# Performance work log

Hardware: AMD Instinct MI355X
Metric: run time of the kernel (lower is better)

The kernel has to match this reference:

```python
import jax, jax.numpy as jnp
import numpy as np

N_NODES = 50000
N_EDGES = 800000
N_FEAT = 128
HIDDEN = 16
N_CLASSES = 16


def spline_conv(x, src, dst, u, weight, root, bias, num_nodes):
    """SplineConv, dim=1, kernel_size=2, degree=1, open spline, aggr='mean'.

    x: [N, in], weight: [2, in, out], u: [E, 1] pseudo-coords in [0, 1).
    Linear B-spline basis over 2 knots: basis = (1-u, u) -> W[0], W[1].
    Transform at node level first (cheaper than per-edge when E > N),
    then gather along edges and scatter-mean to targets.
    """
    h = jnp.einsum('ni,kio->kno', x, weight)  # [2, N, out]
    msg = (1.0 - u) * h[0][src] + u * h[1][src]  # [E, out]
    agg = jax.ops.segment_sum(msg, dst, num_segments=num_nodes)
    deg = jax.ops.segment_sum(jnp.ones((src.shape[0],), x.dtype), dst,
                              num_segments=num_nodes)
    agg = agg / jnp.maximum(deg, 1.0)[:, None]
    return agg + x @ root + bias


def setup_inputs() -> dict:
    key = jax.random.key(0)
    ks = jax.random.split(key, 8)
    x = jax.random.normal(ks[0], (N_NODES, N_FEAT), dtype=jnp.float32)
    edge_index = jax.random.randint(ks[1], (2, N_EDGES), 0, N_NODES, dtype=jnp.int32)
    edge_attr = jax.random.uniform(ks[2], (N_EDGES, 1), dtype=jnp.float32)
    s1 = 1.0 / np.sqrt(N_FEAT)
    s2 = 1.0 / np.sqrt(HIDDEN)
    return {
        'x': x,
        'edge_index': edge_index,
        'edge_attr': edge_attr,
        'w1': jax.random.normal(ks[3], (2, N_FEAT, HIDDEN), dtype=jnp.float32) * s1,
        'root1': jax.random.normal(ks[4], (N_FEAT, HIDDEN), dtype=jnp.float32) * s1,
        'b1': jnp.zeros((HIDDEN,), dtype=jnp.float32),
        'w2': jax.random.normal(ks[5], (2, HIDDEN, N_CLASSES), dtype=jnp.float32) * s2,
        'root2': jax.random.normal(ks[6], (HIDDEN, N_CLASSES), dtype=jnp.float32) * s2,
        'b2': jnp.zeros((N_CLASSES,), dtype=jnp.float32),
    }


def reference(x, edge_index, edge_attr, w1, root1, b1, w2, root2, b2):
    src, dst = edge_index[0], edge_index[1]
    n = x.shape[0]
    # eval mode: F.dropout(training=False) is identity
    h = jax.nn.elu(spline_conv(x, src, dst, edge_attr, w1, root1, b1, n))
    out = spline_conv(h, src, dst, edge_attr, w2, root2, b2, n)
    return jax.nn.log_softmax(out, axis=1)
```

## Files before the change

kernel.cpp:

```cpp
#include <hip/hip_runtime.h>
#include <hip/hip_bf16.h>
#include <math.h>

#define N_NODES 50000
#define N_EDGES 800000
#define N_FEAT 128
#define HIDDEN 16
#define N_CLASSES 16

#define NBUCK 782
#define PB_NB 196
#define PB_E  4096
#define BCAP  1600

typedef __attribute__((ext_vector_type(8))) short short8v;
typedef __attribute__((ext_vector_type(4))) float floatx4;
typedef __attribute__((ext_vector_type(2))) _Float16 half2v;
typedef __attribute__((ext_vector_type(2))) __fp16 fp16x2;

__device__ __forceinline__ unsigned int f2bf_bits(float f) {
    __hip_bfloat16 h = __float2bfloat16(f);
    return (unsigned int)*reinterpret_cast<unsigned short*>(&h);
}
__device__ __forceinline__ half2v cvt_pk(float a, float b) {
    union { fp16x2 f; half2v h; } x;
    x.f = __builtin_amdgcn_cvt_pkrtz(a, b);
    return x.h;
}
__device__ __forceinline__ half2v uint_as_h2(unsigned int v) {
    union { unsigned int u; half2v h; } x; x.u = v; return x.h;
}
__device__ __forceinline__ unsigned int h2_as_uint(half2v h) {
    union { half2v h; unsigned int u; } x; x.h = h; return x.u;
}


__global__ __launch_bounds__(256) void k_node1(
    const float* __restrict__ x, const float* __restrict__ w1,
    const float* __restrict__ root1, const float* __restrict__ b1,
    unsigned int* __restrict__ ABu, float* __restrict__ C,
    int* __restrict__ rank)
{
    if (threadIdx.x == 0) rank[blockIdx.x] = 0;

    int lane = threadIdx.x & 63;
    int wid  = threadIdx.x >> 6;
    int m = lane & 15;
    int q = lane >> 4;
    int nb = blockIdx.x * 64 + wid * 16;

    short8v bf[3][4];
#pragma unroll
    for (int c = 0; c < 4; ++c) {
        int k0 = c * 32 + q * 8;
        const float* p0 = w1 + (size_t)k0 * 16 + m;
        const float* p1 = w1 + 2048 + (size_t)k0 * 16 + m;
        const float* p2 = root1 + (size_t)k0 * 16 + m;
#pragma unroll
        for (int j = 0; j < 8; ++j) {
            bf[0][c][j] = (short)f2bf_bits(p0[j * 16]);
            bf[1][c][j] = (short)f2bf_bits(p1[j * 16]);
            bf[2][c][j] = (short)f2bf_bits(p2[j * 16]);
        }
    }

    int row = min(nb + m, N_NODES - 1);
    const float* xr = x + (size_t)row * N_FEAT;
    short8v af[4];
#pragma unroll
    for (int c = 0; c < 4; ++c) {
        int k0 = c * 32 + q * 8;
        float4 v0 = *(const float4*)(xr + k0);
        float4 v1 = *(const float4*)(xr + k0 + 4);
        af[c][0] = (short)f2bf_bits(v0.x); af[c][1] = (short)f2bf_bits(v0.y);
        af[c][2] = (short)f2bf_bits(v0.z); af[c][3] = (short)f2bf_bits(v0.w);
        af[c][4] = (short)f2bf_bits(v1.x); af[c][5] = (short)f2bf_bits(v1.y);
        af[c][6] = (short)f2bf_bits(v1.z); af[c][7] = (short)f2bf_bits(v1.w);
    }

    floatx4 acc0 = {0.f, 0.f, 0.f, 0.f};
    floatx4 acc1 = {0.f, 0.f, 0.f, 0.f};
    floatx4 acc2 = {0.f, 0.f, 0.f, 0.f};
#pragma unroll
    for (int c = 0; c < 4; ++c) {
        acc0 = __builtin_amdgcn_mfma_f32_16x16x32_bf16(af[c], bf[0][c], acc0, 0, 0, 0);
        acc1 = __builtin_amdgcn_mfma_f32_16x16x32_bf16(af[c], bf[1][c], acc1, 0, 0, 0);
        acc2 = __builtin_amdgcn_mfma_f32_16x16x32_bf16(af[c], bf[2][c], acc2, 0, 0, 0);
    }

    float bo = b1[m];
#pragma unroll
    for (int j = 0; j < 4; ++j) {
        int n = nb + q * 4 + j;
        if (n < N_NODES) {
            ABu[(size_t)n * 16 + m] = h2_as_uint(cvt_pk(acc0[j], acc1[j]));
            C[(size_t)n * 16 + m] = acc2[j] + bo;
        }
    }
}

__global__ __launch_bounds__(256) void k_part(
    const int* __restrict__ src, const int* __restrict__ dst,
    const float* __restrict__ u, int* __restrict__ rank,
    unsigned int* __restrict__ epr)
{
    __shared__ int cnt[NBUCK];
    for (int i = threadIdx.x; i < NBUCK; i += 256) cnt[i] = 0;
    __syncthreads();
    int ebase = blockIdx.x * PB_E;
    int myd[PB_E / 256];
#pragma unroll
    for (int k = 0; k < PB_E / 256; ++k) {
        int e = ebase + k * 256 + threadIdx.x;
        myd[k] = (e < N_EDGES) ? dst[e] : -1;
        if (myd[k] >= 0) atomicAdd(&cnt[myd[k] >> 6], 1);
    }
    __syncthreads();
    for (int i = threadIdx.x; i < NBUCK; i += 256) {
        int c = cnt[i];
        int base = (c > 0) ? atomicAdd(&rank[i], c) : 0;
        cnt[i] = i * BCAP + base;
    }
    __syncthreads();
#pragma unroll
    for (int k = 0; k < PB_E / 256; ++k) {
        if (myd[k] >= 0) {
            int e = ebase + k * 256 + threadIdx.x;
            int b = myd[k] >> 6;
            int pos = atomicAdd(&cnt[b], 1);
            unsigned int u10 = (unsigned int)(u[e] * 1023.f + 0.5f);
            if (pos < (b + 1) * BCAP)
                epr[pos] = ((unsigned int)src[e] & 0xFFFFu)
                         | (((unsigned int)myd[k] & 63u) << 16)
                         | (u10 << 22);
        }
    }
}

__global__ __launch_bounds__(256) void k_bsort(
    const int* __restrict__ rank, const unsigned int* __restrict__ epr,
    unsigned int* __restrict__ epc, unsigned int* __restrict__ rowpack)
{
    __shared__ unsigned int buf[BCAP];
    __shared__ unsigned int sortc[BCAP];
    __shared__ int cnt[64], cur[64];
    int b = blockIdx.x;
    int beg = b * BCAP;
    int m = min(rank[b], BCAP);

    if (threadIdx.x < 64) cnt[threadIdx.x] = 0;
    __syncthreads();
    for (int i = threadIdx.x; i < m; i += 256) {
        unsigned int p = epr[beg + i];
        buf[i] = p;
        atomicAdd(&cnt[(p >> 16) & 63], 1);
    }
    __syncthreads();
    if (threadIdx.x < 64) {
        int v = cnt[threadIdx.x];
        int s = v;
#pragma unroll
        for (int off = 1; off < 64; off <<= 1) {
            int w = __shfl_up(s, off);
            if (threadIdx.x >= off) s += w;
        }
        int ex = s - v;
        cur[threadIdx.x] = ex;
        int n = (b << 6) + threadIdx.x;
        if (n < N_NODES)
            rowpack[n] = (unsigned int)(beg + ex) | ((unsigned int)v << 21);
    }
    __syncthreads();
    for (int i = threadIdx.x; i < m; i += 256) {
        unsigned int p = buf[i];
        int pos = atomicAdd(&cur[(p >> 16) & 63], 1);
        sortc[pos] = p;
    }
    __syncthreads();
    for (int i = threadIdx.x; i < m; i += 256)
        epc[beg + i] = sortc[i];
}

__global__ __launch_bounds__(256) void k_gfused1(
    const unsigned int* __restrict__ rowpack, const unsigned int* __restrict__ ep,
    const unsigned int* __restrict__ ABu, const float* __restrict__ C,
    const float* __restrict__ w2, const float* __restrict__ root2,
    const float* __restrict__ b2,
    unsigned int* __restrict__ ABu2, float* __restrict__ C2)
{
    __shared__ float W2s[16 * 48];
    for (int t = threadIdx.x; t < 16 * 48; t += 256) {
        int j = t / 48, o = t % 48;
        float v;
        if (o < 16)       v = w2[j * 16 + o];
        else if (o < 32)  v = w2[256 + j * 16 + (o - 16)];
        else              v = root2[j * 16 + (o - 32)];
        W2s[t] = v;
    }
    __syncthreads();

    int n    = (blockIdx.x * 256 + threadIdx.x) >> 6;
    int lane = threadIdx.x & 63;
    int g = lane >> 3;
    int l = lane & 7;
    unsigned int rp = rowpack[n];
    int beg = (int)(rp & 0x1FFFFFu);
    int deg = (int)(rp >> 21);
    int end = beg + deg;
    const uint2* AB2 = (const uint2*)ABu;
    const float uscale = 1.f / 1023.f;
    float ax = 0.f, ay = 0.f;
    int e = beg + g;
    for (; e + 8 < end; e += 16) {
        unsigned int p0 = ep[e];
        unsigned int p1 = ep[e + 8];
        float u0 = (float)(p0 >> 22) * uscale;
        float u1 = (float)(p1 >> 22) * uscale;
        half2v w0 = cvt_pk(1.f - u0, u0);
        half2v w1v = cvt_pk(1.f - u1, u1);
        uint2 q0 = AB2[(size_t)(p0 & 0xFFFF) * 8 + l];
        uint2 q1 = AB2[(size_t)(p1 & 0xFFFF) * 8 + l];
        ax = __builtin_amdgcn_fdot2(w0, uint_as_h2(q0.x), ax, false);
        ay = __builtin_amdgcn_fdot2(w0, uint_as_h2(q0.y), ay, false);
        ax = __builtin_amdgcn_fdot2(w1v, uint_as_h2(q1.x), ax, false);
        ay = __builtin_amdgcn_fdot2(w1v, uint_as_h2(q1.y), ay, false);
    }
    if (e < end) {
        unsigned int p0 = ep[e];
        float u0 = (float)(p0 >> 22) * uscale;
        half2v w0 = cvt_pk(1.f - u0, u0);
        uint2 q0 = AB2[(size_t)(p0 & 0xFFFF) * 8 + l];
        ax = __builtin_amdgcn_fdot2(w0, uint_as_h2(q0.x), ax, false);
        ay = __builtin_amdgcn_fdot2(w0, uint_as_h2(q0.y), ay, false);
    }
#pragma unroll
    for (int s = 8; s < 64; s <<= 1) {
        ax += __shfl_xor(ax, s);
        ay += __shfl_xor(ay, s);
    }
    float dv = fmaxf((float)deg, 1.f);
    float2 cv = *(const float2*)&C[(size_t)n * 16 + 2 * l];
    float pre0 = ax / dv + cv.x;
    float pre1 = ay / dv + cv.y;
    float h0 = pre0 > 0.f ? pre0 : expm1f(pre0);
    float h1 = pre1 > 0.f ? pre1 : expm1f(pre1);

    int oc = (lane < 48) ? lane : 0;
    float val = 0.f;
#pragma unroll
    for (int j2 = 0; j2 < 8; ++j2) {
        float hh0 = __shfl(h0, j2);
        float hh1 = __shfl(h1, j2);
        val += hh0 * W2s[(2 * j2) * 48 + oc] + hh1 * W2s[(2 * j2 + 1) * 48 + oc];
    }
    float bval = __shfl(val, (lane + 16) & 63);
    if (lane < 16)
        ABu2[(size_t)n * 16 + lane] = h2_as_uint(cvt_pk(val, bval));
    else if (lane >= 32 && lane < 48)
        C2[(size_t)n * 16 + (lane - 32)] = val + b2[lane - 32];
}

__global__ __launch_bounds__(256) void k_gather2(
    const unsigned int* __restrict__ rowpack, const unsigned int* __restrict__ ep,
    const unsigned int* __restrict__ ABu, const float* __restrict__ C,
    float* __restrict__ out)
{
    int n    = (blockIdx.x * 256 + threadIdx.x) >> 6;
    int lane = threadIdx.x & 63;
    int g = lane >> 3;
    int l = lane & 7;
    unsigned int rp = rowpack[n];
    int beg = (int)(rp & 0x1FFFFFu);
    int deg = (int)(rp >> 21);
    int end = beg + deg;
    const uint2* AB2 = (const uint2*)ABu;
    const float uscale = 1.f / 1023.f;
    float ax = 0.f, ay = 0.f;
    int e = beg + g;
    for (; e + 8 < end; e += 16) {
        unsigned int p0 = ep[e];
        unsigned int p1 = ep[e + 8];
        float u0 = (float)(p0 >> 22) * uscale;
        float u1 = (float)(p1 >> 22) * uscale;
        half2v w0 = cvt_pk(1.f - u0, u0);
        half2v w1v = cvt_pk(1.f - u1, u1);
        uint2 q0 = AB2[(size_t)(p0 & 0xFFFF) * 8 + l];
        uint2 q1 = AB2[(size_t)(p1 & 0xFFFF) * 8 + l];
        ax = __builtin_amdgcn_fdot2(w0, uint_as_h2(q0.x), ax, false);
        ay = __builtin_amdgcn_fdot2(w0, uint_as_h2(q0.y), ay, false);
        ax = __builtin_amdgcn_fdot2(w1v, uint_as_h2(q1.x), ax, false);
        ay = __builtin_amdgcn_fdot2(w1v, uint_as_h2(q1.y), ay, false);
    }
    if (e < end) {
        unsigned int p0 = ep[e];
        float u0 = (float)(p0 >> 22) * uscale;
        half2v w0 = cvt_pk(1.f - u0, u0);
        uint2 q0 = AB2[(size_t)(p0 & 0xFFFF) * 8 + l];
        ax = __builtin_amdgcn_fdot2(w0, uint_as_h2(q0.x), ax, false);
        ay = __builtin_amdgcn_fdot2(w0, uint_as_h2(q0.y), ay, false);
    }
#pragma unroll
    for (int s = 8; s < 64; s <<= 1) {
        ax += __shfl_xor(ax, s);
        ay += __shfl_xor(ay, s);
    }
    float dv = fmaxf((float)deg, 1.f);
    float2 cv = *(const float2*)&C[(size_t)n * 16 + 2 * l];
    float v0 = ax / dv + cv.x;
    float v1 = ay / dv + cv.y;

    float m = fmaxf(v0, v1);
#pragma unroll
    for (int s = 1; s < 8; s <<= 1) m = fmaxf(m, __shfl_xor(m, s));
    float ssum = __expf(v0 - m) + __expf(v1 - m);
#pragma unroll
    for (int s = 1; s < 8; s <<= 1) ssum += __shfl_xor(ssum, s);
    float lse = m + __logf(ssum);
    if (lane < 8)
        *(float2*)&out[(size_t)n * 16 + 2 * l] = make_float2(v0 - lse, v1 - lse);
}

extern "C" void kernel_launch(void* const* d_in, const int* in_sizes, int n_in,
                              void* d_out, int out_size, void* d_ws, size_t ws_size,
                              hipStream_t stream) {
    const float* x     = (const float*)d_in[0];
    const int*   ei    = (const int*)d_in[1];
    const float* ea    = (const float*)d_in[2];
    const float* w1    = (const float*)d_in[3];
    const float* root1 = (const float*)d_in[4];
    const float* b1    = (const float*)d_in[5];
    const float* w2    = (const float*)d_in[6];
    const float* root2 = (const float*)d_in[7];
    const float* b2    = (const float*)d_in[8];
    float* out = (float*)d_out;

    char* ws = (char*)d_ws;
    unsigned int* ABu  = (unsigned int*)ws;
    unsigned int* ABu2 = ABu + (size_t)N_NODES * 16;
    float* C    = (float*)(ABu2 + (size_t)N_NODES * 16);
    float* C2   = C + (size_t)N_NODES * 16;
    unsigned int* EPR = (unsigned int*)(C2 + (size_t)N_NODES * 16);
    unsigned int* EPC = EPR + (size_t)NBUCK * BCAP;
    int* RANK   = (int*)(EPC + (size_t)NBUCK * BCAP);
    unsigned int* ROWPACK = (unsigned int*)(RANK + NBUCK);

    const int* srcp = ei;
    const int* dstp = ei + N_EDGES;

    k_node1<<<782, 256, 0, stream>>>(x, w1, root1, b1, ABu, C, RANK);
    k_part<<<PB_NB, 256, 0, stream>>>(srcp, dstp, ea, RANK, EPR);
    k_bsort<<<NBUCK, 256, 0, stream>>>(RANK, EPR, EPC, ROWPACK);
    k_gfused1<<<N_NODES / 4, 256, 0, stream>>>(ROWPACK, EPC, ABu, C,
                                               w2, root2, b2, ABu2, C2);
    k_gather2<<<N_NODES / 4, 256, 0, stream>>>(ROWPACK, EPC, ABu2, C2, out);
}
```

Measured before the change: 87.43 us.

## Fuse node transform with partitioning and bucket sort with layer-1 gather

Merges the node-level MFMA transform into the edge partition kernel, with only the first blocks doing partitioning, and moves the rank reset to a memset. Bucket sorting is fused with the layer-1 gather/ELU/second transform in one 1024-thread block per bucket, which reads sorted edges straight from shared memory instead of a global round trip. This cuts two launches and some global traffic. In exchange, gather parallelism drops to 782 large blocks, and the partition work now sits in only part of the fused grid.

Result: faster. 80.87 us (-7.5%).

```diff
diff --git a/kernel.cpp b/kernel.cpp
--- a/kernel.cpp
+++ b/kernel.cpp
@@ -35,75 +35,72 @@
 }
 
 
-__global__ __launch_bounds__(256) void k_node1(
+__global__ __launch_bounds__(256) void k_npart(
     const float* __restrict__ x, const float* __restrict__ w1,
     const float* __restrict__ root1, const float* __restrict__ b1,
     unsigned int* __restrict__ ABu, float* __restrict__ C,
-    int* __restrict__ rank)
-{
-    if (threadIdx.x == 0) rank[blockIdx.x] = 0;
-
-    int lane = threadIdx.x & 63;
-    int wid  = threadIdx.x >> 6;
-    int m = lane & 15;
-    int q = lane >> 4;
-    int nb = blockIdx.x * 64 + wid * 16;
-
-    short8v bf[3][4];
-#pragma unroll
-    for (int c = 0; c < 4; ++c) {
-        int k0 = c * 32 + q * 8;
-        const float* p0 = w1 + (size_t)k0 * 16 + m;
-        const float* p1 = w1 + 2048 + (size_t)k0 * 16 + m;
-        const float* p2 = root1 + (size_t)k0 * 16 + m;
-#pragma unroll
-        for (int j = 0; j < 8; ++j) {
-            bf[0][c][j] = (short)f2bf_bits(p0[j * 16]);
-            bf[1][c][j] = (short)f2bf_bits(p1[j * 16]);
-            bf[2][c][j] = (short)f2bf_bits(p2[j * 16]);
-        }
-    }
-
-    int row = min(nb + m, N_NODES - 1);
-    const float* xr = x + (size_t)row * N_FEAT;
-    short8v af[4];
-#pragma unroll
-    for (int c = 0; c < 4; ++c) {
-        int k0 = c * 32 + q * 8;
-        float4 v0 = *(const float4*)(xr + k0);
-        float4 v1 = *(const float4*)(xr + k0 + 4);
-        af[c][0] = (short)f2bf_bits(v0.x); af[c][1] = (short)f2bf_bits(v0.y);
-        af[c][2] = (short)f2bf_bits(v0.z); af[c][3] = (short)f2bf_bits(v0.w);
-        af[c][4] = (short)f2bf_bits(v1.x); af[c][5] = (short)f2bf_bits(v1.y);
-        af[c][6] = (short)f2bf_bits(v1.z); af[c][7] = (short)f2bf_bits(v1.w);
-    }
-
-    floatx4 acc0 = {0.f, 0.f, 0.f, 0.f};
-    floatx4 acc1 = {0.f, 0.f, 0.f, 0.f};
-    floatx4 acc2 = {0.f, 0.f, 0.f, 0.f};
-#pragma unroll
-    for (int c = 0; c < 4; ++c) {
-        acc0 = __builtin_amdgcn_mfma_f32_16x16x32_bf16(af[c], bf[0][c], acc0, 0, 0, 0);
-        acc1 = __builtin_amdgcn_mfma_f32_16x16x32_bf16(af[c], bf[1][c], acc1, 0, 0, 0);
-        acc2 = __builtin_amdgcn_mfma_f32_16x16x32_bf16(af[c], bf[2][c], acc2, 0, 0, 0);
-    }
-
-    float bo = b1[m];
-#pragma unroll
-    for (int j = 0; j < 4; ++j) {
-        int n = nb + q * 4 + j;
-        if (n < N_NODES) {
-            ABu[(size_t)n * 16 + m] = h2_as_uint(cvt_pk(acc0[j], acc1[j]));
-            C[(size_t)n * 16 + m] = acc2[j] + bo;
-        }
-    }
-}
-
-__global__ __launch_bounds__(256) void k_part(
     const int* __restrict__ src, const int* __restrict__ dst,
     const float* __restrict__ u, int* __restrict__ rank,
     unsigned int* __restrict__ epr)
 {
+    {
+        int lane = threadIdx.x & 63;
+        int wid  = threadIdx.x >> 6;
+        int m = lane & 15;
+        int q = lane >> 4;
+        int nb = blockIdx.x * 64 + wid * 16;
+
+        short8v bf[3][4];
+#pragma unroll
+        for (int c = 0; c < 4; ++c) {
+            int k0 = c * 32 + q * 8;
+            const float* p0 = w1 + (size_t)k0 * 16 + m;
+            const float* p1 = w1 + 2048 + (size_t)k0 * 16 + m;
+            const float* p2 = root1 + (size_t)k0 * 16 + m;
+#pragma unroll
+            for (int j = 0; j < 8; ++j) {
+                bf[0][c][j] = (short)f2bf_bits(p0[j * 16]);
+                bf[1][c][j] = (short)f2bf_bits(p1[j * 16]);
+                bf[2][c][j] = (short)f2bf_bits(p2[j * 16]);
+            }
+        }
+
+        int row = min(nb + m, N_NODES - 1);
+        const float* xr = x + (size_t)row * N_FEAT;
+        short8v af[4];
+#pragma unroll
+        for (int c = 0; c < 4; ++c) {
+            int k0 = c * 32 + q * 8;
+            float4 v0 = *(const float4*)(xr + k0);
+            float4 v1 = *(const float4*)(xr + k0 + 4);
+            af[c][0] = (short)f2bf_bits(v0.x); af[c][1] = (short)f2bf_bits(v0.y);
+            af[c][2] = (short)f2bf_bits(v0.z); af[c][3] = (short)f2bf_bits(v0.w);
+            af[c][4] = (short)f2bf_bits(v1.x); af[c][5] = (short)f2bf_bits(v1.y);
+            af[c][6] = (short)f2bf_bits(v1.z); af[c][7] = (short)f2bf_bits(v1.w);
+        }
+
+        floatx4 acc0 = {0.f, 0.f, 0.f, 0.f};
+        floatx4 acc1 = {0.f, 0.f, 0.f, 0.f};
+        floatx4 acc2 = {0.f, 0.f, 0.f, 0.f};
+#pragma unroll
+        for (int c = 0; c < 4; ++c) {
+            acc0 = __builtin_amdgcn_mfma_f32_16x16x32_bf16(af[c], bf[0][c], acc0, 0, 0, 0);
+            acc1 = __builtin_amdgcn_mfma_f32_16x16x32_bf16(af[c], bf[1][c], acc1, 0, 0, 0);
+            acc2 = __builtin_amdgcn_mfma_f32_16x16x32_bf16(af[c], bf[2][c], acc2, 0, 0, 0);
+        }
+
+        float bo = b1[m];
+#pragma unroll
+        for (int j = 0; j < 4; ++j) {
+            int n = nb + q * 4 + j;
+            if (n < N_NODES) {
+                ABu[(size_t)n * 16 + m] = h2_as_uint(cvt_pk(acc0[j], acc1[j]));
+                C[(size_t)n * 16 + m] = acc2[j] + bo;
+            }
+        }
+    }
+
+    if (blockIdx.x >= PB_NB) return;
     __shared__ int cnt[NBUCK];
     for (int i = threadIdx.x; i < NBUCK; i += 256) cnt[i] = 0;
     __syncthreads();
@@ -137,127 +134,131 @@
     }
 }
 
-__global__ __launch_bounds__(256) void k_bsort(
+__global__ __launch_bounds__(1024) void k_sgather(
     const int* __restrict__ rank, const unsigned int* __restrict__ epr,
-    unsigned int* __restrict__ epc, unsigned int* __restrict__ rowpack)
-{
-    __shared__ unsigned int buf[BCAP];
-    __shared__ unsigned int sortc[BCAP];
-    __shared__ int cnt[64], cur[64];
-    int b = blockIdx.x;
-    int beg = b * BCAP;
-    int m = min(rank[b], BCAP);
-
-    if (threadIdx.x < 64) cnt[threadIdx.x] = 0;
-    __syncthreads();
-    for (int i = threadIdx.x; i < m; i += 256) {
-        unsigned int p = epr[beg + i];
-        buf[i] = p;
-        atomicAdd(&cnt[(p >> 16) & 63], 1);
-    }
-    __syncthreads();
-    if (threadIdx.x < 64) {
-        int v = cnt[threadIdx.x];
-        int s = v;
-#pragma unroll
-        for (int off = 1; off < 64; off <<= 1) {
-            int w = __shfl_up(s, off);
-            if (threadIdx.x >= off) s += w;
-        }
-        int ex = s - v;
-        cur[threadIdx.x] = ex;
-        int n = (b << 6) + threadIdx.x;
-        if (n < N_NODES)
-            rowpack[n] = (unsigned int)(beg + ex) | ((unsigned int)v << 21);
-    }
-    __syncthreads();
-    for (int i = threadIdx.x; i < m; i += 256) {
-        unsigned int p = buf[i];
-        int pos = atomicAdd(&cur[(p >> 16) & 63], 1);
-        sortc[pos] = p;
-    }
-    __syncthreads();
-    for (int i = threadIdx.x; i < m; i += 256)
-        epc[beg + i] = sortc[i];
-}
-
-__global__ __launch_bounds__(256) void k_gfused1(
-    const unsigned int* __restrict__ rowpack, const unsigned int* __restrict__ ep,
+    unsigned int* __restrict__ epc, unsigned int* __restrict__ rowpack,
     const unsigned int* __restrict__ ABu, const float* __restrict__ C,
     const float* __restrict__ w2, const float* __restrict__ root2,
     const float* __restrict__ b2,
     unsigned int* __restrict__ ABu2, float* __restrict__ C2)
 {
+    __shared__ unsigned int buf[BCAP];
+    __shared__ unsigned int sorted[BCAP];
+    __shared__ int cnt[64], pre[64], cur[64], degl[64];
     __shared__ float W2s[16 * 48];
-    for (int t = threadIdx.x; t < 16 * 48; t += 256) {
-        int j = t / 48, o = t % 48;
+
+    int t = threadIdx.x;
+    for (int i = t; i < 16 * 48; i += 1024) {
+        int j = i / 48, o = i % 48;
         float v;
         if (o < 16)       v = w2[j * 16 + o];
         else if (o < 32)  v = w2[256 + j * 16 + (o - 16)];
         else              v = root2[j * 16 + (o - 32)];
-        W2s[t] = v;
-    }
-    __syncthreads();
-
-    int n    = (blockIdx.x * 256 + threadIdx.x) >> 6;
-    int lane = threadIdx.x & 63;
+        W2s[i] = v;
+    }
+    int b = blockIdx.x;
+    int beg = b * BCAP;
+    int m = min(rank[b], BCAP);
+    if (t < 64) cnt[t] = 0;
+    __syncthreads();
+
+    for (int i = t; i < m; i += 1024) {
+        unsigned int p = epr[beg + i];
+        buf[i] = p;
+        atomicAdd(&cnt[(p >> 16) & 63], 1);
+    }
+    __syncthreads();
+    if (t < 64) {
+        int v = cnt[t];
+        int s = v;
+#pragma unroll
+        for (int off = 1; off < 64; off <<= 1) {
+            int w = __shfl_up(s, off);
+            if (t >= off) s += w;
+        }
+        int ex = s - v;
+        pre[t] = ex;
+        cur[t] = ex;
+        degl[t] = v;
+        int n = (b << 6) + t;
+        if (n < N_NODES)
+            rowpack[n] = (unsigned int)(beg + ex) | ((unsigned int)v << 21);
+    }
+    __syncthreads();
+    for (int i = t; i < m; i += 1024) {
+        unsigned int p = buf[i];
+        int pos = atomicAdd(&cur[(p >> 16) & 63], 1);
+        sorted[pos] = p;
+    }
+    __syncthreads();
+    for (int i = t; i < m; i += 1024)
+        epc[beg + i] = sorted[i];
+
+    int wv = t >> 6;
+    int lane = t & 63;
     int g = lane >> 3;
     int l = lane & 7;
-    unsigned int rp = rowpack[n];
-    int beg = (int)(rp & 0x1FFFFFu);
-    int deg = (int)(rp >> 21);
-    int end = beg + deg;
     const uint2* AB2 = (const uint2*)ABu;
     const float uscale = 1.f / 1023.f;
-    float ax = 0.f, ay = 0.f;
-    int e = beg + g;
-    for (; e + 8 < end; e += 16) {
-        unsigned int p0 = ep[e];
-        unsigned int p1 = ep[e + 8];
-        float u0 = (float)(p0 >> 22) * uscale;
-        float u1 = (float)(p1 >> 22) * uscale;
-        half2v w0 = cvt_pk(1.f - u0, u0);
-        half2v w1v = cvt_pk(1.f - u1, u1);
-        uint2 q0 = AB2[(size_t)(p0 & 0xFFFF) * 8 + l];
-        uint2 q1 = AB2[(size_t)(p1 & 0xFFFF) * 8 + l];
-        ax = __builtin_amdgcn_fdot2(w0, uint_as_h2(q0.x), ax, false);
-        ay = __builtin_amdgcn_fdot2(w0, uint_as_h2(q0.y), ay, false);
-        ax = __builtin_amdgcn_fdot2(w1v, uint_as_h2(q1.x), ax, false);
-        ay = __builtin_amdgcn_fdot2(w1v, uint_as_h2(q1.y), ay, false);
-    }
-    if (e < end) {
-        unsigned int p0 = ep[e];
-        float u0 = (float)(p0 >> 22) * uscale;
-        half2v w0 = cvt_pk(1.f - u0, u0);
-        uint2 q0 = AB2[(size_t)(p0 & 0xFFFF) * 8 + l];
-        ax = __builtin_amdgcn_fdot2(w0, uint_as_h2(q0.x), ax, false);
-        ay = __builtin_amdgcn_fdot2(w0, uint_as_h2(q0.y), ay, false);
-    }
-#pragma unroll
-    for (int s = 8; s < 64; s <<= 1) {
-        ax += __shfl_xor(ax, s);
-        ay += __shfl_xor(ay, s);
-    }
-    float dv = fmaxf((float)deg, 1.f);
-    float2 cv = *(const float2*)&C[(size_t)n * 16 + 2 * l];
-    float pre0 = ax / dv + cv.x;
-    float pre1 = ay / dv + cv.y;
-    float h0 = pre0 > 0.f ? pre0 : expm1f(pre0);
-    float h1 = pre1 > 0.f ? pre1 : expm1f(pre1);
-
-    int oc = (lane < 48) ? lane : 0;
-    float val = 0.f;
-#pragma unroll
-    for (int j2 = 0; j2 < 8; ++j2) {
-        float hh0 = __shfl(h0, j2);
-        float hh1 = __shfl(h1, j2);
-        val += hh0 * W2s[(2 * j2) * 48 + oc] + hh1 * W2s[(2 * j2 + 1) * 48 + oc];
-    }
-    float bval = __shfl(val, (lane + 16) & 63);
-    if (lane < 16)
-        ABu2[(size_t)n * 16 + lane] = h2_as_uint(cvt_pk(val, bval));
-    else if (lane >= 32 && lane < 48)
-        C2[(size_t)n * 16 + (lane - 32)] = val + b2[lane - 32];
+
+#pragma unroll
+    for (int j = 0; j < 4; ++j) {
+        int nl = wv * 4 + j;
+        int n = (b << 6) + nl;
+        if (n >= N_NODES) break;
+        int begL = pre[nl];
+        int deg  = degl[nl];
+        int endL = begL + deg;
+        float ax = 0.f, ay = 0.f;
+        int e = begL + g;
+        for (; e + 8 < endL; e += 16) {
+            unsigned int p0 = sorted[e];
+            unsigned int p1 = sorted[e + 8];
+            float u0 = (float)(p0 >> 22) * uscale;
+            float u1 = (float)(p1 >> 22) * uscale;
+            half2v w0 = cvt_pk(1.f - u0, u0);
+            half2v w1v = cvt_pk(1.f - u1, u1);
+            uint2 q0 = AB2[(size_t)(p0 & 0xFFFF) * 8 + l];
+            uint2 q1 = AB2[(size_t)(p1 & 0xFFFF) * 8 + l];
+            ax = __builtin_amdgcn_fdot2(w0, uint_as_h2(q0.x), ax, false);
+            ay = __builtin_amdgcn_fdot2(w0, uint_as_h2(q0.y), ay, false);
+            ax = __builtin_amdgcn_fdot2(w1v, uint_as_h2(q1.x), ax, false);
+            ay = __builtin_amdgcn_fdot2(w1v, uint_as_h2(q1.y), ay, false);
+        }
+        if (e < endL) {
+            unsigned int p0 = sorted[e];
+            float u0 = (float)(p0 >> 22) * uscale;
+            half2v w0 = cvt_pk(1.f - u0, u0);
+            uint2 q0 = AB2[(size_t)(p0 & 0xFFFF) * 8 + l];
+            ax = __builtin_amdgcn_fdot2(w0, uint_as_h2(q0.x), ax, false);
+            ay = __builtin_amdgcn_fdot2(w0, uint_as_h2(q0.y), ay, false);
+        }
+#pragma unroll
+        for (int s = 8; s < 64; s <<= 1) {
+            ax += __shfl_xor(ax, s);
+            ay += __shfl_xor(ay, s);
+        }
+        float dv = fmaxf((float)deg, 1.f);
+        float2 cv = *(const float2*)&C[(size_t)n * 16 + 2 * l];
+        float pre0 = ax / dv + cv.x;
+        float pre1 = ay / dv + cv.y;
+        float h0 = pre0 > 0.f ? pre0 : expm1f(pre0);
+        float h1 = pre1 > 0.f ? pre1 : expm1f(pre1);
+
+        int oc = (lane < 48) ? lane : 0;
+        float val = 0.f;
+#pragma unroll
+        for (int j2 = 0; j2 < 8; ++j2) {
+            float hh0 = __shfl(h0, j2);
+            float hh1 = __shfl(h1, j2);
+            val += hh0 * W2s[(2 * j2) * 48 + oc] + hh1 * W2s[(2 * j2 + 1) * 48 + oc];
+        }
+        float bval = __shfl(val, (lane + 16) & 63);
+        if (lane < 16)
+            ABu2[(size_t)n * 16 + lane] = h2_as_uint(cvt_pk(val, bval));
+        else if (lane >= 32 && lane < 48)
+            C2[(size_t)n * 16 + (lane - 32)] = val + b2[lane - 32];
+    }
 }
 
 __global__ __launch_bounds__(256) void k_gather2(
@@ -347,10 +348,11 @@
     const int* srcp = ei;
     const int* dstp = ei + N_EDGES;
 
-    k_node1<<<782, 256, 0, stream>>>(x, w1, root1, b1, ABu, C, RANK);
-    k_part<<<PB_NB, 256, 0, stream>>>(srcp, dstp, ea, RANK, EPR);
-    k_bsort<<<NBUCK, 256, 0, stream>>>(RANK, EPR, EPC, ROWPACK);
-    k_gfused1<<<N_NODES / 4, 256, 0, stream>>>(ROWPACK, EPC, ABu, C,
-                                               w2, root2, b2, ABu2, C2);
+    hipMemsetAsync(RANK, 0, NBUCK * sizeof(int), stream);
+
+    k_npart<<<782, 256, 0, stream>>>(x, w1, root1, b1, ABu, C,
+                                     srcp, dstp, ea, RANK, EPR);
+    k_sgather<<<NBUCK, 1024, 0, stream>>>(RANK, EPR, EPC, ROWPACK, ABu, C,
+                                          w2, root2, b2, ABu2, C2);
     k_gather2<<<N_NODES / 4, 256, 0, stream>>>(ROWPACK, EPC, ABu2, C2, out);
 }
```
